# Optimization experiments

Measured on AMD Instinct MI355X. Metric: run time of the kernel, lower is better.

The kernel has to match this reference:

```python
import jax, jax.numpy as jnp
import numpy as np

N_NODES = 50000
N_EDGES = 800000
N_GRAPHS = 128
IN_CH, HIDDEN, OUT_CH = 16, 64, 2


def gcn_conv(x, src, dst, W, b, n_nodes):
    """GCNConv: add self-loops, sym-normalized adjacency scatter-add, linear."""
    h = x @ W  # [N, H]
    loop = jnp.arange(n_nodes, dtype=src.dtype)
    s = jnp.concatenate([src, loop])  # [E+N]
    d = jnp.concatenate([dst, loop])
    deg = jax.ops.segment_sum(jnp.ones_like(d, dtype=h.dtype), d, num_segments=n_nodes)
    dinv = jnp.where(deg > 0, jax.lax.rsqrt(deg), 0.0)  # deg^{-1/2}
    norm = dinv[s] * dinv[d]  # [E+N]
    msg = h[s] * norm[:, None]  # gather + scale, [E+N, H]
    out = jax.ops.segment_sum(msg, d, num_segments=n_nodes)  # scatter-add
    return out + b


def global_mean_pool(x, batch, n_graphs):
    sums = jax.ops.segment_sum(x, batch, num_segments=n_graphs)
    cnts = jax.ops.segment_sum(jnp.ones((x.shape[0],), x.dtype), batch, num_segments=n_graphs)
    return sums / jnp.maximum(cnts, 1.0)[:, None]


def setup_inputs() -> dict:
    key = jax.random.key(0)
    ks = jax.random.split(key, 10)
    x = jax.random.normal(ks[0], (N_NODES, IN_CH), dtype=jnp.float32)
    edge_index = jax.random.randint(ks[1], (2, N_EDGES), 0, N_NODES, dtype=jnp.int64)
    batch = jnp.sort(jax.random.randint(ks[2], (N_NODES,), 0, N_GRAPHS, dtype=jnp.int64))
    def glorot(k, shp):
        lim = float(np.sqrt(6.0 / (shp[0] + shp[1])))
        return jax.random.uniform(k, shp, jnp.float32, -lim, lim)
    W1 = glorot(ks[3], (IN_CH, HIDDEN))
    b1 = jnp.zeros((HIDDEN,), jnp.float32)
    W2 = glorot(ks[4], (HIDDEN, HIDDEN))
    b2 = jnp.zeros((HIDDEN,), jnp.float32)
    Wc = glorot(ks[5], (HIDDEN, OUT_CH))
    bc = jnp.zeros((OUT_CH,), jnp.float32)
    return {"x": x, "edge_index": edge_index, "batch": batch,
            "W1": W1, "b1": b1, "W2": W2, "b2": b2, "Wc": Wc, "bc": bc}


def reference(x, edge_index, batch, W1, b1, W2, b2, Wc, bc):
    src, dst = edge_index[0], edge_index[1]
    n = x.shape[0]
    h = jax.nn.relu(gcn_conv(x, src, dst, W1, b1, n))
    # dropout p=0.3 is identity in eval mode
    h = jax.nn.relu(gcn_conv(h, src, dst, W2, b2, n))
    g = global_mean_pool(h, batch, N_GRAPHS)  # [G, H]
    return g @ Wc + bc  # [G, out_channels]
```

## Files before the change

kernel.cpp:

```cpp
#include <hip/hip_runtime.h>
#include <hip/hip_bf16.h>

#define N_NODES 50000
#define N_EDGES 800000
#define N_GRAPHS 128
#define IN_CH 16
#define HIDDEN 64
#define OUT_CH 2

#define BSHIFT 7
#define BNODES 128
#define NB ((N_NODES + BNODES - 1) / BNODES)
#define BCAP 3072
#define ECHUNK 4096
#define EB ((N_EDGES + ECHUNK - 1) / ECHUNK)
#define MAXK 12
#define WT1_LD 18
#define AGG_LD 72
#define W2T_ENT (HIDDEN * AGG_LD)

typedef __attribute__((ext_vector_type(8))) short bf16x8;
typedef __attribute__((ext_vector_type(4))) float f32x4;

__device__ __forceinline__ float bf2f(unsigned short u) {
    return __uint_as_float(((unsigned)u) << 16);
}
__device__ __forceinline__ unsigned short f2bf(float f) {
    __hip_bfloat16 h = __float2bfloat16(f);
    return *reinterpret_cast<unsigned short*>(&h);
}


__global__ void init_kernel(int* __restrict__ zbase, int zwords,
                            const float* __restrict__ W2, unsigned short* __restrict__ w2t) {
    int gid = blockIdx.x * 256 + threadIdx.x;
    int gsz = gridDim.x * 256;
    for (int i = gid; i < zwords; i += gsz) zbase[i] = 0;
    for (int i = gid; i < HIDDEN * HIDDEN; i += gsz) {
        int k = i >> 6, c = i & 63;
        w2t[c * AGG_LD + k] = f2bf(W2[i]);
    }
}


__global__ void bucket_scatter_kernel(const int* __restrict__ src, const int* __restrict__ dst,
                                      int* __restrict__ bcnt, int* __restrict__ pairs) {
    __shared__ int lcnt[NB];
    __shared__ int goff[NB];
    __shared__ int lcur[NB];
    int t = threadIdx.x;
    for (int i = t; i < NB; i += 256) lcnt[i] = 0;
    __syncthreads();
    int base = blockIdx.x * ECHUNK;
    for (int i = t; i < ECHUNK; i += 256) {
        int e = base + i;
        if (e < N_EDGES) {
            int d = dst[e];
            if ((unsigned)d < N_NODES) atomicAdd(&lcnt[d >> BSHIFT], 1);
        }
    }
    __syncthreads();
    for (int i = t; i < NB; i += 256) {
        int c = lcnt[i];
        goff[i] = (c > 0) ? atomicAdd(&bcnt[i], c) : 0;
        lcur[i] = 0;
    }
    __syncthreads();
    for (int i = t; i < ECHUNK; i += 256) {
        int e = base + i;
        if (e < N_EDGES) {
            int d = dst[e];
            if ((unsigned)d < N_NODES) {
                int b = d >> BSHIFT;
                int r = goff[b] + atomicAdd(&lcur[b], 1);
                if (r < BCAP) pairs[b * BCAP + r] = (src[e] << BSHIFT) | (d & (BNODES - 1));
            }
        }
    }
}

__global__ void bucket_csr_kernel(const int* __restrict__ pairs, const int* __restrict__ bcnt,
                                  int* __restrict__ csr, int* __restrict__ rowptr,
                                  int* __restrict__ cnt_node, float* __restrict__ dinv,
                                  const float* __restrict__ x, float* __restrict__ xs) {
    __shared__ int lcnt[BNODES];
    __shared__ int ls[BNODES];
    __shared__ int lrow[BNODES];
    __shared__ float sdv[BNODES];
    int b = blockIdx.x;
    int t = threadIdx.x;
    if (t < BNODES) lcnt[t] = 0;
    __syncthreads();
    int bstart = b * BCAP;
    int K = bcnt[b];
    if (K > BCAP) K = BCAP;
    int myp[MAXK], myr[MAXK];
#pragma unroll
    for (int k = 0; k < MAXK; k++) {
        int i = k * 256 + t;
        if (i < K) {
            int p = pairs[bstart + i];
            myp[k] = p;
            myr[k] = atomicAdd(&lcnt[p & (BNODES - 1)], 1);
        }
    }
    __syncthreads();
    if (t < BNODES) ls[t] = lcnt[t];
    __syncthreads();
    for (int off = 1; off < BNODES; off <<= 1) {
        int u = (t >= off && t < BNODES) ? ls[t - off] : 0;
        __syncthreads();
        if (t < BNODES) ls[t] += u;
        __syncthreads();
    }
    if (t < BNODES) {
        int ex = ls[t] - lcnt[t];
        lrow[t] = ex;
        float dv = rsqrtf((float)(lcnt[t] + 1));
        sdv[t] = dv;
        int n = b * BNODES + t;
        if (n < N_NODES) {
            rowptr[n] = bstart + ex;
            cnt_node[n] = lcnt[t];
            dinv[n] = dv;
        }
    }
    __syncthreads();
#pragma unroll
    for (int k = 0; k < MAXK; k++) {
        int i = k * 256 + t;
        if (i < K) csr[bstart + lrow[myp[k] & (BNODES - 1)] + myr[k]] = myp[k] >> BSHIFT;
    }
    for (int i = t; i < BNODES * IN_CH; i += 256) {
        int nl = i >> 4;
        int n = b * BNODES + nl;
        if (n < N_NODES) xs[n * IN_CH + (i & 15)] = sdv[nl] * x[n * IN_CH + (i & 15)];
    }
}


__global__ void fused_l1_kernel(const float* __restrict__ xs, const int* __restrict__ csr_src,
                                const int* __restrict__ rowptr, const int* __restrict__ cnt,
                                const float* __restrict__ dinv, const float* __restrict__ W,
                                const float* __restrict__ b, __hip_bfloat16* __restrict__ h) {
    __shared__ float sWT[HIDDEN * WT1_LD];
    __shared__ float sx[16 * IN_CH];
    int t = threadIdx.x;
    for (int i = t; i < IN_CH * HIDDEN; i += 256) {
        int k = i >> 6, c = i & 63;
        sWT[c * WT1_LD + k] = W[i];
    }

    int n0 = blockIdx.x * 16;
    int w = t >> 6;
    int lane = t & 63;
    int e16 = lane >> 2;
    int cc = (lane & 3) * 4;

    int lens[4], starts[4];
#pragma unroll
    for (int q = 0; q < 4; q++) {
        int n = n0 + w * 4 + q;
        lens[q] = cnt[n];
        starts[q] = rowptr[n];
    }

    for (int q = 0; q < 4; q++) {
        int row = w * 4 + q;
        int n = n0 + row;
        int len = lens[q];
        int start = starts[q];
        int last = len - 1;
        int iters = (len + 31) >> 5;
        float4 acc = make_float4(0.f, 0.f, 0.f, 0.f);
        for (int m = 0; m < iters; m++) {
            int base = m * 32 + e16;
#pragma unroll
            for (int k = 0; k < 2; k++) {
                int j = base + 16 * k;
                int jj = j <= last ? j : last;
                float msk = j <= last ? 1.0f : 0.0f;
                int s = csr_src[start + jj];
                float4 xv = *(const float4*)&xs[s * IN_CH + cc];
                acc.x += msk * xv.x; acc.y += msk * xv.y;
                acc.z += msk * xv.z; acc.w += msk * xv.w;
            }
        }
#pragma unroll
        for (int m = 4; m <= 32; m <<= 1) {
            acc.x += __shfl_xor(acc.x, m, 64);
            acc.y += __shfl_xor(acc.y, m, 64);
            acc.z += __shfl_xor(acc.z, m, 64);
            acc.w += __shfl_xor(acc.w, m, 64);
        }
        if (lane < 4) {
            float dn = dinv[n];
            float4 xsv = *(const float4*)&xs[n * IN_CH + cc];
            float4 v;
            v.x = dn * (acc.x + xsv.x);
            v.y = dn * (acc.y + xsv.y);
            v.z = dn * (acc.z + xsv.z);
            v.w = dn * (acc.w + xsv.w);
            *(float4*)&sx[row * IN_CH + cc] = v;
        }
    }
    __syncthreads();

    int r = w;
    int c = t & 63;
    float bias = b[c];
#pragma unroll
    for (int nb = 0; nb < 4; nb++) {
        int row = nb * 4 + r;
        int n = n0 + row;
        if (n >= N_NODES) continue;
        float acch = bias;
#pragma unroll
        for (int k4 = 0; k4 < IN_CH; k4 += 4) {
            float4 a = *(const float4*)&sx[row * IN_CH + k4];
            float2 w0 = *(const float2*)&sWT[c * WT1_LD + k4];
            float2 w1 = *(const float2*)&sWT[c * WT1_LD + k4 + 2];
            acch += a.x * w0.x + a.y * w0.y + a.z * w1.x + a.w * w1.y;
        }
        float v = acch > 0.0f ? acch : 0.0f;
        h[n * HIDDEN + c] = __float2bfloat16(dinv[n] * v);
    }
}


__global__ void fused_l2_kernel(const __hip_bfloat16* __restrict__ h, const int* __restrict__ csr_src,
                                const int* __restrict__ rowptr, const int* __restrict__ cnt,
                                const float* __restrict__ dinv, const unsigned short* __restrict__ w2t,
                                const float* __restrict__ b, const int* __restrict__ batch,
                                float* __restrict__ sums, float* __restrict__ cntg) {
    __shared__ unsigned short sW[W2T_ENT];
    __shared__ unsigned short sagg[16 * AGG_LD];
    int t = threadIdx.x;
    {
        const uint4* wp = (const uint4*)w2t;
        uint4* sWv = (uint4*)sW;
#pragma unroll
        for (int i = 0; i < 3; i++) {
            int idx = i * 256 + t;
            if (idx < W2T_ENT / 8) sWv[idx] = wp[idx];
        }
    }

    int n0 = blockIdx.x * 16;
    int w = t >> 6;
    int lane = t & 63;
    int e8 = lane >> 3;
    int cc8 = (lane & 7) * 8;
    const unsigned short* hu = (const unsigned short*)h;

    int lens[4], starts[4];
#pragma unroll
    for (int q = 0; q < 4; q++) {
        int n = n0 + w * 4 + q;
        lens[q] = cnt[n];
        starts[q] = rowptr[n];
    }

    for (int q = 0; q < 4; q++) {
        int row = w * 4 + q;
        int n = n0 + row;
        int len = lens[q];
        int start = starts[q];
        int last = len - 1;
        int iters = (len + 31) >> 5;
        float4 alo = make_float4(0.f, 0.f, 0.f, 0.f);
        float4 ahi = make_float4(0.f, 0.f, 0.f, 0.f);
        for (int m = 0; m < iters; m++) {
            int base = m * 32 + e8;
#pragma unroll
            for (int k = 0; k < 4; k++) {
                int j = base + 8 * k;
                int jj = j <= last ? j : last;
                float msk = j <= last ? 1.0f : 0.0f;
                int s = csr_src[start + jj];
                uint4 raw = *(const uint4*)&hu[s * HIDDEN + cc8];
                alo.x += msk * __uint_as_float(raw.x << 16);
                alo.y += msk * __uint_as_float(raw.x & 0xffff0000u);
                alo.z += msk * __uint_as_float(raw.y << 16);
                alo.w += msk * __uint_as_float(raw.y & 0xffff0000u);
                ahi.x += msk * __uint_as_float(raw.z << 16);
                ahi.y += msk * __uint_as_float(raw.z & 0xffff0000u);
                ahi.z += msk * __uint_as_float(raw.w << 16);
                ahi.w += msk * __uint_as_float(raw.w & 0xffff0000u);
            }
        }
#pragma unroll
        for (int m = 8; m <= 32; m <<= 1) {
            alo.x += __shfl_xor(alo.x, m, 64);
            alo.y += __shfl_xor(alo.y, m, 64);
            alo.z += __shfl_xor(alo.z, m, 64);
            alo.w += __shfl_xor(alo.w, m, 64);
            ahi.x += __shfl_xor(ahi.x, m, 64);
            ahi.y += __shfl_xor(ahi.y, m, 64);
            ahi.z += __shfl_xor(ahi.z, m, 64);
            ahi.w += __shfl_xor(ahi.w, m, 64);
        }
        if (lane < 8) {
            uint4 sv = *(const uint4*)&hu[n * HIDDEN + cc8];
            float dn = dinv[n];
            ushort4 o0, o1;
            o0.x = f2bf(dn * (alo.x + __uint_as_float(sv.x << 16)));
            o0.y = f2bf(dn * (alo.y + __uint_as_float(sv.x & 0xffff0000u)));
            o0.z = f2bf(dn * (alo.z + __uint_as_float(sv.y << 16)));
            o0.w = f2bf(dn * (alo.w + __uint_as_float(sv.y & 0xffff0000u)));
            o1.x = f2bf(dn * (ahi.x + __uint_as_float(sv.z << 16)));
            o1.y = f2bf(dn * (ahi.y + __uint_as_float(sv.z & 0xffff0000u)));
            o1.z = f2bf(dn * (ahi.z + __uint_as_float(sv.w << 16)));
            o1.w = f2bf(dn * (ahi.w + __uint_as_float(sv.w & 0xffff0000u)));
            *(ushort4*)&sagg[row * AGG_LD + cc8] = o0;
            *(ushort4*)&sagg[row * AGG_LD + cc8 + 4] = o1;
        }
    }
    __syncthreads();

    int quad = lane >> 4;
    int col = lane & 15;
    int cch = w * 16 + col;
    bf16x8 a0 = *(const bf16x8*)&sagg[col * AGG_LD + quad * 8];
    bf16x8 a1 = *(const bf16x8*)&sagg[col * AGG_LD + 32 + quad * 8];
    bf16x8 b0 = *(const bf16x8*)&sW[cch * AGG_LD + quad * 8];
    bf16x8 b1 = *(const bf16x8*)&sW[cch * AGG_LD + 32 + quad * 8];
    f32x4 d = {0.f, 0.f, 0.f, 0.f};
    d = __builtin_amdgcn_mfma_f32_16x16x32_bf16(a0, b0, d, 0, 0, 0);
    d = __builtin_amdgcn_mfma_f32_16x16x32_bf16(a1, b1, d, 0, 0, 0);
    float bias = b[cch];
    float v[4];
#pragma unroll
    for (int r = 0; r < 4; r++) {
        float z = d[r] + bias;
        v[r] = z > 0.0f ? z : 0.0f;
    }

    int glo = batch[n0];
    int ghi = batch[n0 + 15];
    if (glo == ghi) {
        float s4 = (v[0] + v[1]) + (v[2] + v[3]);
        s4 += __shfl_xor(s4, 16, 64);
        s4 += __shfl_xor(s4, 32, 64);
        if (quad == 0) atomicAdd(&sums[glo * HIDDEN + cch], s4);
        if (t == 0) atomicAdd(&cntg[glo], 16.0f);
    } else {
#pragma unroll
        for (int r = 0; r < 4; r++) {
            int g = batch[n0 + quad * 4 + r];
            if ((unsigned)g < N_GRAPHS) atomicAdd(&sums[g * HIDDEN + cch], v[r]);
        }
        if (w == 0 && col == 0) {
#pragma unroll
            for (int r = 0; r < 4; r++) {
                int g = batch[n0 + quad * 4 + r];
                if ((unsigned)g < N_GRAPHS) atomicAdd(&cntg[g], 1.0f);
            }
        }
    }
}


__global__ void head_kernel(const float* __restrict__ sums, const float* __restrict__ cntg,
                            const float* __restrict__ Wc, const float* __restrict__ bc,
                            float* __restrict__ out) {
    int t = blockIdx.x * blockDim.x + threadIdx.x;
    if (t >= N_GRAPHS * OUT_CH) return;
    int g = t >> 1;
    int o = t & 1;
    float inv = 1.0f / fmaxf(cntg[g], 1.0f);
    float acc = bc[o];
#pragma unroll
    for (int k = 0; k < HIDDEN; k++) acc += sums[g * HIDDEN + k] * inv * Wc[k * OUT_CH + o];
    out[t] = acc;
}


extern "C" void kernel_launch(void* const* d_in, const int* in_sizes, int n_in,
                              void* d_out, int out_size, void* d_ws, size_t ws_size,
                              hipStream_t stream) {
    const float* x  = (const float*)d_in[0];
    const int* ei   = (const int*)d_in[1];
    const int* bat  = (const int*)d_in[2];
    const float* W1 = (const float*)d_in[3];
    const float* b1 = (const float*)d_in[4];
    const float* W2 = (const float*)d_in[5];
    const float* b2 = (const float*)d_in[6];
    const float* Wc = (const float*)d_in[7];
    const float* bc = (const float*)d_in[8];
    float* out = (float*)d_out;

    const int* src = ei;
    const int* dst = ei + N_EDGES;

    char* ws = (char*)d_ws;
    size_t off = 0;
    auto carve = [&](size_t nbytes) {
        char* p = ws + off;
        off += (nbytes + 255) & ~(size_t)255;
        return p;
    };
    float* sums     = (float*)carve(N_GRAPHS * HIDDEN * sizeof(float));
    float* cntg     = (float*)carve(N_GRAPHS * sizeof(float));
    int*   bcnt     = (int*)carve(NB * sizeof(int));
    size_t zeroBytes = off;
    unsigned short* w2t = (unsigned short*)carve(W2T_ENT * sizeof(unsigned short));
    int*   pairs    = (int*)carve((size_t)NB * BCAP * sizeof(int));
    int*   csr      = (int*)carve((size_t)NB * BCAP * sizeof(int));
    int*   rowptr   = (int*)carve(N_NODES * sizeof(int));
    int*   cnt_node = (int*)carve(N_NODES * sizeof(int));
    float* dinv     = (float*)carve(N_NODES * sizeof(float));
    float* xs       = (float*)carve((size_t)N_NODES * IN_CH * sizeof(float));
    __hip_bfloat16* bufA = (__hip_bfloat16*)carve((size_t)N_NODES * HIDDEN * sizeof(__hip_bfloat16));
    (void)ws_size;

    const int node16Blk = (N_NODES + 15) / 16;

    init_kernel<<<32, 256, 0, stream>>>((int*)sums, (int)(zeroBytes / 4), W2, w2t);
    bucket_scatter_kernel<<<EB, 256, 0, stream>>>(src, dst, bcnt, pairs);
    bucket_csr_kernel<<<NB, 256, 0, stream>>>(pairs, bcnt, csr, rowptr, cnt_node, dinv, x, xs);

    fused_l1_kernel<<<node16Blk, 256, 0, stream>>>(xs, csr, rowptr, cnt_node, dinv, W1, b1, bufA);
    fused_l2_kernel<<<node16Blk, 256, 0, stream>>>(bufA, csr, rowptr, cnt_node, dinv, w2t, b2,
                                                   bat, sums, cntg);
    head_kernel<<<1, 256, 0, stream>>>(sums, cntg, Wc, bc, out);
}
```

Measured before the change: 167.6 us.

## Remove init and head kernels, replace global bucket atomics with per-chunk histograms

Folds the W2 transpose into the scatter kernel, moves zeroing of pooled sums into the CSR kernel, and fuses the classifier head into the layer-2 kernel through a last-block-done counter. This cuts the launch count from six to four. The bucket scatter stops taking global atomic slots per bucket and instead writes per-chunk histograms and chunk-local sorted pairs. The CSR kernel then prefix-scans those histograms and binary-searches each segment to gather its bucket's pairs. This trades global atomics and two launches for extra scan and search work in the CSR kernel, plus a threadfence and counter at the end of layer 2.

```diff
diff --git a/kernel.cpp b/kernel.cpp
--- a/kernel.cpp
+++ b/kernel.cpp
@@ -15,6 +15,7 @@
 #define ECHUNK 4096
 #define EB ((N_EDGES + ECHUNK - 1) / ECHUNK)
 #define MAXK 12
+#define EPT 16
 #define WT1_LD 18
 #define AGG_LD 72
 #define W2T_ENT (HIDDEN * AGG_LD)
@@ -31,90 +32,145 @@
 }
 
 
-__global__ void init_kernel(int* __restrict__ zbase, int zwords,
-                            const float* __restrict__ W2, unsigned short* __restrict__ w2t) {
-    int gid = blockIdx.x * 256 + threadIdx.x;
-    int gsz = gridDim.x * 256;
-    for (int i = gid; i < zwords; i += gsz) zbase[i] = 0;
-    for (int i = gid; i < HIDDEN * HIDDEN; i += gsz) {
-        int k = i >> 6, c = i & 63;
-        w2t[c * AGG_LD + k] = f2bf(W2[i]);
-    }
-}
-
-
 __global__ void bucket_scatter_kernel(const int* __restrict__ src, const int* __restrict__ dst,
-                                      int* __restrict__ bcnt, int* __restrict__ pairs) {
-    __shared__ int lcnt[NB];
-    __shared__ int goff[NB];
-    __shared__ int lcur[NB];
+                                      int* __restrict__ bh, int* __restrict__ bh2,
+                                      int* __restrict__ pairs,
+                                      const float* __restrict__ W2, unsigned short* __restrict__ w2t) {
+    __shared__ int lh[NB];
+    __shared__ int lstart[NB];
+    __shared__ int spair[256];
     int t = threadIdx.x;
-    for (int i = t; i < NB; i += 256) lcnt[i] = 0;
-    __syncthreads();
+    if (blockIdx.x == 0) {
+        for (int i = t; i < HIDDEN * HIDDEN; i += 256) {
+            int k = i >> 6, c = i & 63;
+            w2t[c * AGG_LD + k] = f2bf(W2[i]);
+        }
+    }
+    for (int i = t; i < NB; i += 256) lh[i] = 0;
+    __syncthreads();
+
     int base = blockIdx.x * ECHUNK;
-    for (int i = t; i < ECHUNK; i += 256) {
-        int e = base + i;
-        if (e < N_EDGES) {
-            int d = dst[e];
-            if ((unsigned)d < N_NODES) atomicAdd(&lcnt[d >> BSHIFT], 1);
-        }
-    }
-    __syncthreads();
+    int nE = N_EDGES - base;
+    if (nE > ECHUNK) nE = ECHUNK;
+
+    int ed[EPT], es[EPT];
+#pragma unroll
+    for (int k = 0; k < EPT; k++) {
+        int i = k * 256 + t;
+        if (i < nE) {
+            ed[k] = dst[base + i];
+            es[k] = src[base + i];
+        } else {
+            ed[k] = -1;
+            es[k] = 0;
+        }
+    }
+#pragma unroll
+    for (int k = 0; k < EPT; k++)
+        if ((unsigned)ed[k] < N_NODES) atomicAdd(&lh[ed[k] >> BSHIFT], 1);
+    __syncthreads();
+
+    int a0 = (2 * t < NB) ? lh[2 * t] : 0;
+    int a1 = (2 * t + 1 < NB) ? lh[2 * t + 1] : 0;
+    spair[t] = a0 + a1;
+    __syncthreads();
+    for (int off = 1; off < 256; off <<= 1) {
+        int u = (t >= off) ? spair[t - off] : 0;
+        __syncthreads();
+        spair[t] += u;
+        __syncthreads();
+    }
+    int ex = spair[t] - (a0 + a1);
+    if (2 * t < NB) lstart[2 * t] = ex;
+    if (2 * t + 1 < NB) lstart[2 * t + 1] = ex + a0;
+    __syncthreads();
+
     for (int i = t; i < NB; i += 256) {
-        int c = lcnt[i];
-        goff[i] = (c > 0) ? atomicAdd(&bcnt[i], c) : 0;
-        lcur[i] = 0;
-    }
-    __syncthreads();
-    for (int i = t; i < ECHUNK; i += 256) {
-        int e = base + i;
-        if (e < N_EDGES) {
-            int d = dst[e];
-            if ((unsigned)d < N_NODES) {
-                int b = d >> BSHIFT;
-                int r = goff[b] + atomicAdd(&lcur[b], 1);
-                if (r < BCAP) pairs[b * BCAP + r] = (src[e] << BSHIFT) | (d & (BNODES - 1));
-            }
-        }
-    }
-}
-
-__global__ void bucket_csr_kernel(const int* __restrict__ pairs, const int* __restrict__ bcnt,
+        bh[i * EB + blockIdx.x] = lh[i];
+        bh2[i * EB + blockIdx.x] = base + lstart[i];
+        lh[i] = 0;
+    }
+    __syncthreads();
+
+#pragma unroll
+    for (int k = 0; k < EPT; k++) {
+        if ((unsigned)ed[k] < N_NODES) {
+            int b = ed[k] >> BSHIFT;
+            int r = atomicAdd(&lh[b], 1);
+            pairs[base + lstart[b] + r] = (es[k] << BSHIFT) | (ed[k] & (BNODES - 1));
+        }
+    }
+}
+
+
+__global__ void bucket_csr_kernel(const int* __restrict__ pairs, const int* __restrict__ bh,
+                                  const int* __restrict__ bh2,
                                   int* __restrict__ csr, int* __restrict__ rowptr,
                                   int* __restrict__ cnt_node, float* __restrict__ dinv,
-                                  const float* __restrict__ x, float* __restrict__ xs) {
+                                  const float* __restrict__ x, float* __restrict__ xs,
+                                  float* __restrict__ sums, float* __restrict__ cntg,
+                                  int* __restrict__ done) {
+    __shared__ int segaddr[EB];
+    __shared__ int pref[EB];
+    __shared__ int ptmp[256];
     __shared__ int lcnt[BNODES];
-    __shared__ int ls[BNODES];
+    __shared__ int lsc[BNODES];
     __shared__ int lrow[BNODES];
     __shared__ float sdv[BNODES];
     int b = blockIdx.x;
     int t = threadIdx.x;
+
+    if (b == 0) {
+        for (int i = t; i < N_GRAPHS * HIDDEN; i += 256) sums[i] = 0.0f;
+        if (t < N_GRAPHS) cntg[t] = 0.0f;
+        if (t == 0) *done = 0;
+    }
+
+    int cntv = (t < EB) ? bh[b * EB + t] : 0;
+    if (t < EB) segaddr[t] = bh2[b * EB + t];
     if (t < BNODES) lcnt[t] = 0;
-    __syncthreads();
-    int bstart = b * BCAP;
-    int K = bcnt[b];
+    ptmp[t] = cntv;
+    __syncthreads();
+    for (int off = 1; off < 256; off <<= 1) {
+        int u = (t >= off) ? ptmp[t - off] : 0;
+        __syncthreads();
+        ptmp[t] += u;
+        __syncthreads();
+    }
+    if (t < EB) pref[t] = ptmp[t];
+    __syncthreads();
+    int K = pref[EB - 1];
     if (K > BCAP) K = BCAP;
+
     int myp[MAXK], myr[MAXK];
 #pragma unroll
     for (int k = 0; k < MAXK; k++) {
         int i = k * 256 + t;
+        myp[k] = -1;
         if (i < K) {
-            int p = pairs[bstart + i];
+            int lo = 0, hi = EB - 1;
+            while (lo < hi) {
+                int mid = (lo + hi) >> 1;
+                if (pref[mid] > i) hi = mid; else lo = mid + 1;
+            }
+            int excl = (lo > 0) ? pref[lo - 1] : 0;
+            int p = pairs[segaddr[lo] + (i - excl)];
             myp[k] = p;
             myr[k] = atomicAdd(&lcnt[p & (BNODES - 1)], 1);
         }
     }
     __syncthreads();
-    if (t < BNODES) ls[t] = lcnt[t];
+    if (t < BNODES) lsc[t] = lcnt[t];
     __syncthreads();
     for (int off = 1; off < BNODES; off <<= 1) {
-        int u = (t >= off && t < BNODES) ? ls[t - off] : 0;
-        __syncthreads();
-        if (t < BNODES) ls[t] += u;
-        __syncthreads();
-    }
+        int u = (t >= off && t < BNODES) ? lsc[t - off] : 0;
+        __syncthreads();
+        if (t < BNODES) lsc[t] += u;
+        __syncthreads();
+    }
+    int bstart = b * BCAP;
     if (t < BNODES) {
-        int ex = ls[t] - lcnt[t];
+        int ex = lsc[t] - lcnt[t];
         lrow[t] = ex;
         float dv = rsqrtf((float)(lcnt[t] + 1));
         sdv[t] = dv;
@@ -128,8 +184,8 @@
     __syncthreads();
 #pragma unroll
     for (int k = 0; k < MAXK; k++) {
-        int i = k * 256 + t;
-        if (i < K) csr[bstart + lrow[myp[k] & (BNODES - 1)] + myr[k]] = myp[k] >> BSHIFT;
+        if (myp[k] >= 0)
+            csr[bstart + lrow[myp[k] & (BNODES - 1)] + myr[k]] = myp[k] >> BSHIFT;
     }
     for (int i = t; i < BNODES * IN_CH; i += 256) {
         int nl = i >> 4;
@@ -232,9 +288,12 @@
                                 const int* __restrict__ rowptr, const int* __restrict__ cnt,
                                 const float* __restrict__ dinv, const unsigned short* __restrict__ w2t,
                                 const float* __restrict__ b, const int* __restrict__ batch,
-                                float* __restrict__ sums, float* __restrict__ cntg) {
+                                float* __restrict__ sums, float* __restrict__ cntg,
+                                int* __restrict__ done, const float* __restrict__ Wc,
+                                const float* __restrict__ bc, float* __restrict__ out) {
     __shared__ unsigned short sW[W2T_ENT];
     __shared__ unsigned short sagg[16 * AGG_LD];
+    __shared__ int lastFlag;
     int t = threadIdx.x;
     {
         const uint4* wp = (const uint4*)w2t;
@@ -358,21 +417,27 @@
             }
         }
     }
-}
-
-
-__global__ void head_kernel(const float* __restrict__ sums, const float* __restrict__ cntg,
-                            const float* __restrict__ Wc, const float* __restrict__ bc,
-                            float* __restrict__ out) {
-    int t = blockIdx.x * blockDim.x + threadIdx.x;
-    if (t >= N_GRAPHS * OUT_CH) return;
-    int g = t >> 1;
-    int o = t & 1;
-    float inv = 1.0f / fmaxf(cntg[g], 1.0f);
-    float acc = bc[o];
-#pragma unroll
-    for (int k = 0; k < HIDDEN; k++) acc += sums[g * HIDDEN + k] * inv * Wc[k * OUT_CH + o];
-    out[t] = acc;
+
+    __threadfence();
+    __syncthreads();
+    if (t == 0) lastFlag = (atomicAdd(done, 1) == (int)gridDim.x - 1) ? 1 : 0;
+    __syncthreads();
+    if (lastFlag) {
+        for (int i = t; i < N_GRAPHS * OUT_CH; i += 256) {
+            int g = i >> 1;
+            int o = i & 1;
+            float cg = __hip_atomic_load(&cntg[g], __ATOMIC_RELAXED, __HIP_MEMORY_SCOPE_AGENT);
+            float inv = 1.0f / fmaxf(cg, 1.0f);
+            float acc = bc[o];
+#pragma unroll
+            for (int k = 0; k < HIDDEN; k++) {
+                float sv = __hip_atomic_load(&sums[g * HIDDEN + k], __ATOMIC_RELAXED,
+                                             __HIP_MEMORY_SCOPE_AGENT);
+                acc += sv * inv * Wc[k * OUT_CH + o];
+            }
+            out[i] = acc;
+        }
+    }
 }
 
 
@@ -402,10 +467,11 @@
     };
     float* sums     = (float*)carve(N_GRAPHS * HIDDEN * sizeof(float));
     float* cntg     = (float*)carve(N_GRAPHS * sizeof(float));
-    int*   bcnt     = (int*)carve(NB * sizeof(int));
-    size_t zeroBytes = off;
+    int*   done     = (int*)carve(sizeof(int));
     unsigned short* w2t = (unsigned short*)carve(W2T_ENT * sizeof(unsigned short));
-    int*   pairs    = (int*)carve((size_t)NB * BCAP * sizeof(int));
+    int*   bh       = (int*)carve((size_t)NB * EB * sizeof(int));
+    int*   bh2      = (int*)carve((size_t)NB * EB * sizeof(int));
+    int*   pairs    = (int*)carve((size_t)EB * ECHUNK * sizeof(int));
     int*   csr      = (int*)carve((size_t)NB * BCAP * sizeof(int));
     int*   rowptr   = (int*)carve(N_NODES * sizeof(int));
     int*   cnt_node = (int*)carve(N_NODES * sizeof(int));
@@ -416,12 +482,10 @@
 
     const int node16Blk = (N_NODES + 15) / 16;
 
-    init_kernel<<<32, 256, 0, stream>>>((int*)sums, (int)(zeroBytes / 4), W2, w2t);
-    bucket_scatter_kernel<<<EB, 256, 0, stream>>>(src, dst, bcnt, pairs);
-    bucket_csr_kernel<<<NB, 256, 0, stream>>>(pairs, bcnt, csr, rowptr, cnt_node, dinv, x, xs);
-
+    bucket_scatter_kernel<<<EB, 256, 0, stream>>>(src, dst, bh, bh2, pairs, W2, w2t);
+    bucket_csr_kernel<<<NB, 256, 0, stream>>>(pairs, bh, bh2, csr, rowptr, cnt_node, dinv,
+                                              x, xs, sums, cntg, done);
     fused_l1_kernel<<<node16Blk, 256, 0, stream>>>(xs, csr, rowptr, cnt_node, dinv, W1, b1, bufA);
     fused_l2_kernel<<<node16Blk, 256, 0, stream>>>(bufA, csr, rowptr, cnt_node, dinv, w2t, b2,
-                                                   bat, sums, cntg);
-    head_kernel<<<1, 256, 0, stream>>>(sums, cntg, Wc, bc, out);
-}
+                                                   bat, sums, cntg, done, Wc, bc, out);
+}
```

Measured after the change: 389.1 us. 2.32x slower.
